# Kernel tuning notes

Hardware: AMD Instinct MI355X
Metric: run time of the kernel (lower is better)

The kernel has to match this reference:

```python
import jax, jax.numpy as jnp
import numpy as np

NUM_GRAPHS = 512
N_NODES = 131072
N_EDGES = 4194304
F_IN = 54
H_GCN = 16
H_LSTM = 32
N_CLASSES = 192
MAX_SEQ_LEN = 1024


def setup_inputs() -> dict:
    key = jax.random.key(0)
    ks = jax.random.split(key, 12)
    s = 0.1
    return {
        "x": jax.random.normal(ks[0], (N_NODES, F_IN), jnp.float32),
        "edge_index": jax.random.randint(ks[1], (2, N_EDGES), 0, N_NODES),
        "batch": jnp.sort(jax.random.randint(ks[2], (N_NODES,), 0, NUM_GRAPHS)),
        "gcn_w1": jax.random.normal(ks[3], (F_IN, H_GCN), jnp.float32) * s,
        "gcn_b1": jnp.zeros((H_GCN,), jnp.float32),
        "gcn_w2": jax.random.normal(ks[4], (H_GCN, H_GCN), jnp.float32) * s,
        "gcn_b2": jnp.zeros((H_GCN,), jnp.float32),
        "lstm0_wih": jax.random.normal(ks[5], (2, 4 * H_LSTM, H_GCN), jnp.float32) * s,
        "lstm0_whh": jax.random.normal(ks[6], (2, 4 * H_LSTM, H_LSTM), jnp.float32) * s,
        "lstm0_bih": jnp.zeros((2, 4 * H_LSTM), jnp.float32),
        "lstm0_bhh": jnp.zeros((2, 4 * H_LSTM), jnp.float32),
        "lstm1_wih": jax.random.normal(ks[7], (2, 4 * H_LSTM, 2 * H_LSTM), jnp.float32) * s,
        "lstm1_whh": jax.random.normal(ks[8], (2, 4 * H_LSTM, H_LSTM), jnp.float32) * s,
        "lstm1_bih": jnp.zeros((2, 4 * H_LSTM), jnp.float32),
        "lstm1_bhh": jnp.zeros((2, 4 * H_LSTM), jnp.float32),
        "fc_w": jax.random.normal(ks[9], (2 * H_LSTM, N_CLASSES), jnp.float32) * s,
        "fc_b": jnp.zeros((N_CLASSES,), jnp.float32),
        "max_seq_len": MAX_SEQ_LEN,
    }


def _lstm_dir(xseq, wih, whh, bih, bhh, reverse):
    # xseq: [B, T, D]; PyTorch gate order i, f, g, o.
    pre = jnp.einsum("btd,gd->btg", xseq, wih) + bih + bhh  # [B, T, 4H]
    B = xseq.shape[0]
    H = whh.shape[-1]

    def step(carry, g_t):
        h, c = carry
        g = g_t + h @ whh.T
        i, f, gg, o = jnp.split(g, 4, axis=-1)
        c = jax.nn.sigmoid(f) * c + jax.nn.sigmoid(i) * jnp.tanh(gg)
        h = jax.nn.sigmoid(o) * jnp.tanh(c)
        return (h, c), h

    init = (jnp.zeros((B, H), xseq.dtype), jnp.zeros((B, H), xseq.dtype))
    _, hs = jax.lax.scan(step, init, jnp.swapaxes(pre, 0, 1), reverse=reverse)
    return jnp.swapaxes(hs, 0, 1)  # [B, T, H]


def _bilstm(xseq, wih, whh, bih, bhh):
    fwd = _lstm_dir(xseq, wih[0], whh[0], bih[0], bhh[0], reverse=False)
    bwd = _lstm_dir(xseq, wih[1], whh[1], bih[1], bhh[1], reverse=True)
    return jnp.concatenate([fwd, bwd], axis=-1)


def reference(x, edge_index, batch, gcn_w1, gcn_b1, gcn_w2, gcn_b2,
              lstm0_wih, lstm0_whh, lstm0_bih, lstm0_bhh,
              lstm1_wih, lstm1_whh, lstm1_bih, lstm1_bhh,
              fc_w, fc_b, max_seq_len):
    N = x.shape[0]
    loop = jnp.arange(N)
    src = jnp.concatenate([edge_index[0], loop])  # GCNConv adds self-loops
    dst = jnp.concatenate([edge_index[1], loop])
    deg = jax.ops.segment_sum(jnp.ones_like(dst, jnp.float32), dst, num_segments=N)
    dinv = jax.lax.rsqrt(jnp.maximum(deg, 1.0))  # deg >= 1 due to self-loops
    norm = (dinv[src] * dinv[dst])[:, None]

    def conv(h, W, b):
        msg = (h @ W)[src] * norm
        return jax.ops.segment_sum(msg, dst, num_segments=N) + b

    h = jax.nn.relu(conv(x, gcn_w1, gcn_b1))
    # F.dropout(training=False) is identity in eval mode
    h = jax.nn.relu(conv(h, gcn_w2, gcn_b2))

    # Ragged -> padded [NUM_GRAPHS, max_seq_len, H_GCN] (batch is graph-sorted)
    counts = jax.ops.segment_sum(jnp.ones((N,), jnp.int32), batch, num_segments=NUM_GRAPHS)
    starts = jnp.concatenate([jnp.zeros((1,), jnp.int32), jnp.cumsum(counts)[:-1]])
    pos = jnp.arange(N) - starts[batch]
    padded = jnp.zeros((NUM_GRAPHS, max_seq_len, h.shape[1]), h.dtype).at[batch, pos].set(h, mode="drop")

    seq = _bilstm(padded, lstm0_wih, lstm0_whh, lstm0_bih, lstm0_bhh)
    seq = _bilstm(seq, lstm1_wih, lstm1_whh, lstm1_bih, lstm1_bhh)
    pooled = jnp.mean(seq, axis=1)  # mean over padded length, as in original
    return pooled @ fc_w + fc_b
```

## Files before the change

### kernel.cpp

```cpp
#include <hip/hip_runtime.h>
#include <cstdint>
#include <cstddef>

#define NG 512
#define NN 131072
#define NE 4194304
#define FIN 54
#define HG 16
#define HL 32
#define NC 192
#define TS 1024

#define NB 256
#define WH 512
#define EPW (NE/WH)

__device__ __forceinline__ float rcpf(float x){ return __builtin_amdgcn_rcpf(x); }
__device__ __forceinline__ float sigf(float x){ return rcpf(1.0f + __expf(-x)); }
__device__ __forceinline__ float tanhfast(float x){ return 1.0f - 2.0f*rcpf(__expf(2.0f*x) + 1.0f); }

__device__ __forceinline__ float4 uload4(const float* p){
  unsigned long long a = (unsigned long long)p;
  asm volatile("" : "+v"(a));
  return *(const float4*)a;
}

#define CEPS 1e-6f
#define HEPS 1e-6f

__global__ void k_initc(int* __restrict__ counts){
  counts[threadIdx.x] = 0;
}

__global__ void k_cnt(const int* __restrict__ batch, int* __restrict__ counts){
  int i = blockIdx.x*256 + threadIdx.x;
  if (i < NN) atomicAdd(&counts[batch[i]], 1);
}

__global__ void k_scan(const int* __restrict__ counts, int* __restrict__ starts){
  __shared__ int sc[NG];
  int t = threadIdx.x;
  sc[t] = counts[t]; __syncthreads();
  for (int off = 1; off < NG; off <<= 1){
    int v = (t >= off) ? sc[t-off] : 0;
    __syncthreads();
    sc[t] += v;
    __syncthreads();
  }
  starts[t] = sc[t] - counts[t];
}

__global__ void k_hist(const int* __restrict__ ei, int* __restrict__ hist){
  int w = blockIdx.x, tid = threadIdx.x;
  __shared__ int h[NB];
  h[tid] = 0;
  __syncthreads();
  int e0 = w*EPW;
  for (int i = tid; i < EPW; i += 256) atomicAdd(&h[ei[NE + e0 + i] >> 9], 1);
  __syncthreads();
  hist[tid*WH + w] = h[tid];
}

__global__ void k_scanH(const int* __restrict__ hist, int* __restrict__ offs,
                        int* __restrict__ bstart){
  __shared__ int tot[1024];
  int t = threadIdx.x;
  int base = t*128;
  int s = 0;
  for (int i = 0; i < 128; i++) s += hist[base + i];
  tot[t] = s; __syncthreads();
  for (int o = 1; o < 1024; o <<= 1){
    int v = (t >= o) ? tot[t-o] : 0;
    __syncthreads();
    tot[t] += v;
    __syncthreads();
  }
  int run = tot[t] - s;
  for (int i = 0; i < 128; i++){
    int idx = base + i;
    int h = hist[idx];
    offs[idx] = run;
    if ((idx & (WH-1)) == 0) bstart[idx / WH] = run;
    run += h;
  }
  if (t == 0) bstart[NB] = NE;
}

__global__ void k_binB(const int* __restrict__ ei, const int* __restrict__ offs,
                       uint2* __restrict__ pair){
  int w = blockIdx.x, tid = threadIdx.x;
  __shared__ int cur[NB];
  cur[tid] = offs[tid*WH + w];
  __syncthreads();
  int e0 = w*EPW;
  for (int i = tid; i < EPW; i += 256){
    int e = e0 + i;
    int s = ei[e], d = ei[NE + e];
    int b = d >> 9;
    int pos = atomicAdd(&cur[b], 1);
    pair[pos] = make_uint2((unsigned)s, (unsigned)(d & 511));
  }
}

__global__ void k_binC(const uint2* __restrict__ pair, const int* __restrict__ bstart,
                       int* __restrict__ eoff, int* __restrict__ ecnt, int* __restrict__ csr){
  int b = blockIdx.x, tid = threadIdx.x;
  __shared__ int h2[512];
  __shared__ int cur[512];
  h2[tid] = 0; h2[tid + 256] = 0;
  __syncthreads();
  int e0 = bstart[b], e1 = bstart[b+1];
  for (int i = e0 + tid; i < e1; i += 256) atomicAdd(&h2[pair[i].y], 1);
  __syncthreads();
  cur[tid] = h2[tid]; cur[tid + 256] = h2[tid + 256];
  __syncthreads();
  for (int o = 1; o < 256; o <<= 1){
    int v0 = (tid >= o) ? cur[tid - o] : 0;
    int v1 = (tid >= o) ? cur[256 + tid - o] : 0;
    __syncthreads();
    cur[tid] += v0; cur[256 + tid] += v1;
    __syncthreads();
  }
  int half0 = cur[255];
  __syncthreads();
  cur[256 + tid] += half0;
  __syncthreads();
  int n0 = tid, n1 = tid + 256;
  int ex0 = cur[n0] - h2[n0];
  int ex1 = cur[n1] - h2[n1];
  eoff[b*512 + n0] = e0 + ex0; ecnt[b*512 + n0] = h2[n0];
  eoff[b*512 + n1] = e0 + ex1; ecnt[b*512 + n1] = h2[n1];
  __syncthreads();
  cur[n0] = e0 + ex0; cur[n1] = e0 + ex1;
  __syncthreads();
  for (int i = e0 + tid; i < e1; i += 256){
    uint2 u = pair[i];
    int pos = atomicAdd(&cur[u.y], 1);
    csr[pos] = (int)u.x;
  }
}

__global__ void k_dinv(const int* __restrict__ ecnt, float* __restrict__ dinv){
  int i = blockIdx.x*256 + threadIdx.x;
  if (i < NN) dinv[i] = 1.0f / sqrtf((float)(ecnt[i] + 1));
}

__global__ void k_lin1(const float* __restrict__ x, const float* __restrict__ w1,
                       float* __restrict__ xa){
  __shared__ float w[FIN*HG];
  __shared__ float xs[16][FIN+2];
  int tid = threadIdx.x;
  for (int i = tid; i < FIN*HG; i += 256) w[i] = w1[i];
  const float4* gx = (const float4*)(x + (size_t)blockIdx.x*16*FIN);
  if (tid < 216){
    float4 v4 = gx[tid];
    int fi = tid*4;
#pragma unroll
    for (int e = 0; e < 4; e++){
      int idx = fi + e;
      xs[idx/FIN][idx%FIN] = ((const float*)&v4)[e];
    }
  }
  __syncthreads();
  int node = tid >> 4, f = tid & 15;
  const float* xr = xs[node];
  float acc = 0.0f;
#pragma unroll
  for (int k = 0; k < FIN; k++) acc = fmaf(xr[k], w[k*HG + f], acc);
  xa[((size_t)blockIdx.x*16 + node)*HG + f] = acc;
}

__global__ void k_gather(const float* __restrict__ v, const int* __restrict__ csr,
                         const int* __restrict__ eoff, const int* __restrict__ ecnt,
                         const float* __restrict__ dinv, const float* __restrict__ bias,
                         int dorelu, float* __restrict__ out){
  int gid = blockIdx.x*16 + (threadIdx.x >> 4);
  int f = threadIdx.x & 15;
  float dv = dinv[gid];
  float a0 = v[(size_t)gid*HG + f] * dv, a1 = 0.0f, a2 = 0.0f, a3 = 0.0f;
  int o = eoff[gid], n = ecnt[gid];
  int i = 0;
  for (; i + 8 <= n; i += 8){
    int s0 = csr[o+i],   s1 = csr[o+i+1], s2 = csr[o+i+2], s3 = csr[o+i+3];
    int s4 = csr[o+i+4], s5 = csr[o+i+5], s6 = csr[o+i+6], s7 = csr[o+i+7];
    a0 = fmaf(v[(size_t)s0*HG + f], dinv[s0], a0);
    a1 = fmaf(v[(size_t)s1*HG + f], dinv[s1], a1);
    a2 = fmaf(v[(size_t)s2*HG + f], dinv[s2], a2);
    a3 = fmaf(v[(size_t)s3*HG + f], dinv[s3], a3);
    a0 = fmaf(v[(size_t)s4*HG + f], dinv[s4], a0);
    a1 = fmaf(v[(size_t)s5*HG + f], dinv[s5], a1);
    a2 = fmaf(v[(size_t)s6*HG + f], dinv[s6], a2);
    a3 = fmaf(v[(size_t)s7*HG + f], dinv[s7], a3);
  }
  for (; i + 4 <= n; i += 4){
    int s0 = csr[o+i], s1 = csr[o+i+1], s2 = csr[o+i+2], s3 = csr[o+i+3];
    a0 = fmaf(v[(size_t)s0*HG + f], dinv[s0], a0);
    a1 = fmaf(v[(size_t)s1*HG + f], dinv[s1], a1);
    a2 = fmaf(v[(size_t)s2*HG + f], dinv[s2], a2);
    a3 = fmaf(v[(size_t)s3*HG + f], dinv[s3], a3);
  }
  for (; i < n; i++){
    int s = csr[o+i];
    a0 = fmaf(v[(size_t)s*HG + f], dinv[s], a0);
  }
  float acc = ((a0 + a1) + (a2 + a3)) * dv;
  if (dorelu) acc = fmaxf(acc + bias[f], 0.0f);
  out[(size_t)gid*HG + f] = acc;
}

__global__ void k_relu_lin(const float* __restrict__ agg, const float* __restrict__ b1,
                           const float* __restrict__ w2, float* __restrict__ hb){
  __shared__ float w[HG*HG];
  __shared__ float bb[HG];
  int tid = threadIdx.x;
  if (tid < HG*HG) w[tid] = w2[tid];
  if (tid < HG) bb[tid] = b1[tid];
  __syncthreads();
  int id = blockIdx.x*256 + tid;
  if (id >= NN*HG) return;
  int node = id >> 4, f = id & 15;
  const float* ar = agg + (size_t)node*HG;
  float acc = 0.0f;
#pragma unroll
  for (int k = 0; k < HG; k++){
    float h = fmaxf(ar[k] + bb[k], 0.0f);
    acc = fmaf(h, w[k*HG + f], acc);
  }
  hb[id] = acc;
}


__global__ __launch_bounds__(64, 1) void k_lstm0(
    const float* __restrict__ h2in, const int* __restrict__ starts, const int* __restrict__ counts,
    const float* __restrict__ wih, const float* __restrict__ whh,
    const float* __restrict__ bih, const float* __restrict__ bhh,
    float* __restrict__ out0, int* __restrict__ tconv, int* __restrict__ az)
{
  const int g = blockIdx.x >> 1, dir = blockIdx.x & 1;
  const int lane = threadIdx.x;
  const int j = lane & 31, half = lane >> 5;
  const int rA = (half ? 32 : 0) + j;
  const int rB = rA + 64;
  float wxA[HG], wxB[HG], whA[HL], whB[HL];
  { const float* a = wih + ((size_t)dir*128 + rA)*HG;
    const float* b = wih + ((size_t)dir*128 + rB)*HG;
#pragma unroll
    for (int k = 0; k < HG; k++){ wxA[k] = a[k]; wxB[k] = b[k]; }
    const float* ua = whh + ((size_t)dir*128 + rA)*HL;
    const float* ub = whh + ((size_t)dir*128 + rB)*HL;
#pragma unroll
    for (int k = 0; k < HL; k++){ whA[k] = ua[k]; whB[k] = ub[k]; }
  }
  const float pbA = bih[dir*128 + rA] + bhh[dir*128 + rA];
  const float pbB = bih[dir*128 + rB] + bhh[dir*128 + rB];
  int cnt = counts[g]; if (cnt > TS) cnt = TS;
  const int s0 = starts[g];
  float* outg = out0 + (size_t)g*TS*64 + dir*32;

  __shared__ __align__(16) float hbuf[HL];

  unsigned long long bz = __ballot((pbA == 0.0f) && (pbB == 0.0f));
  bool allzero = (bz == ~0ull);
  if (dir == 1 && lane == 0) az[0] = allzero ? 1 : 0;
  if (!half) hbuf[j] = 0.0f;

  int t0, dt; bool skipall = false;
  if (dir == 0){ t0 = 0; dt = 1; }
  else if (allzero){
    t0 = cnt - 1; dt = -1;
    if (t0 < 0) skipall = true;
  } else { t0 = TS - 1; dt = -1; }

  float c = 0.0f, h = 0.0f; bool fwdconv = false;
  float4 X[4]; int t = t0;

  if (!skipall){
    if (cnt > 0){
      int ta = t0 < 0 ? 0 : (t0 > cnt-1 ? cnt-1 : t0);
      const float* pa = h2in + (size_t)(s0 + ta)*HG;
#pragma unroll
      for (int q = 0; q < 4; q++) X[q] = uload4(pa + 4*q);
    }
    for (;;){
      float a0 = pbA, a1 = 0.0f, a2 = 0.0f, a3 = 0.0f;
      float b0 = pbB, b1 = 0.0f, b2 = 0.0f, b3 = 0.0f;
      if (t < cnt){
#pragma unroll
        for (int q = 0; q < 4; q++){ float4 xq = X[q];
          a0 = fmaf(xq.x, wxA[4*q+0], a0); a1 = fmaf(xq.y, wxA[4*q+1], a1);
          a2 = fmaf(xq.z, wxA[4*q+2], a2); a3 = fmaf(xq.w, wxA[4*q+3], a3);
          b0 = fmaf(xq.x, wxB[4*q+0], b0); b1 = fmaf(xq.y, wxB[4*q+1], b1);
          b2 = fmaf(xq.z, wxB[4*q+2], b2); b3 = fmaf(xq.w, wxB[4*q+3], b3); }
      }
      { int tp = t + dt;
        if (tp >= 0 && tp < cnt){
          const float* pp = h2in + (size_t)(s0 + tp)*HG;
#pragma unroll
          for (int q = 0; q < 4; q++) X[q] = uload4(pp + 4*q);
        } }
      { const float4* h4 = (const float4*)hbuf;
#pragma unroll
        for (int q = 0; q < HL/4; q++){ float4 hq = h4[q];
          a0 = fmaf(hq.x, whA[4*q+0], a0); a1 = fmaf(hq.y, whA[4*q+1], a1);
          a2 = fmaf(hq.z, whA[4*q+2], a2); a3 = fmaf(hq.w, whA[4*q+3], a3);
          b0 = fmaf(hq.x, whB[4*q+0], b0); b1 = fmaf(hq.y, whB[4*q+1], b1);
          b2 = fmaf(hq.z, whB[4*q+2], b2); b3 = fmaf(hq.w, whB[4*q+3], b3); }
      }
      float uA = (a0 + a1) + (a2 + a3);
      float uB = (b0 + b1) + (b2 + b3);
      float aA = sigf(uA);
      float ub2 = half ? uB : (uB + uB);
      float sv = sigf(ub2);
      float aB = half ? sv : (sv + sv - 1.0f);
      float pq = aA*aB;
      float part = __shfl_xor(half ? aA : pq, 32);
      float f_ = half ? aA : part;
      float p_ = half ? part : pq;
      float cn = fmaf(f_, c, p_);
      float th = tanhfast(cn);
      float ov = __shfl_xor(aB, 32);
      float o_ = half ? aB : ov;
      float hn = o_ * th;
      bool eq = (fabsf(cn - c) <= CEPS*(1.0f + fabsf(cn))) && (fabsf(hn - h) <= HEPS);
      c = cn; h = hn;
      unsigned long long m = __ballot(eq);
      if (!half) hbuf[j] = h;
      if (half) outg[(size_t)t*64 + j] = h;
      if (dir == 0 && t >= cnt + 1 && m == ~0ull){
        if (lane == 0) tconv[g] = t - 1;
        fwdconv = true;
        break;
      }
      t += dt;
      if (dir == 0){ if (t >= TS) break; } else { if (t < 0) break; }
    }
  }
  if (dir == 0 && !fwdconv && lane == 0) tconv[g] = TS;
}

__global__ __launch_bounds__(64, 1) void k_lstm1(
    const float* __restrict__ gl0, const int* __restrict__ tconv,
    const int* __restrict__ counts, const int* __restrict__ az,
    const float* __restrict__ wih, const float* __restrict__ whh,
    const float* __restrict__ bih, const float* __restrict__ bhh,
    float* __restrict__ pooled)
{
  const int g = blockIdx.x >> 1, dir = blockIdx.x & 1;
  const int lane = threadIdx.x;
  const int j = lane & 31, half = lane >> 5;
  const int rA = (half ? 32 : 0) + j, rB = rA + 64;
  float wxA[64], wxB[64], whA[HL], whB[HL];
  { const float4* A4 = (const float4*)(wih + ((size_t)dir*128 + rA)*64);
    const float4* B4 = (const float4*)(wih + ((size_t)dir*128 + rB)*64);
#pragma unroll
    for (int k = 0; k < 16; k++){ ((float4*)wxA)[k] = A4[k]; ((float4*)wxB)[k] = B4[k]; }
    const float4* a4 = (const float4*)(whh + ((size_t)dir*128 + rA)*HL);
    const float4* b4 = (const float4*)(whh + ((size_t)dir*128 + rB)*HL);
#pragma unroll
    for (int k = 0; k < 8; k++){ ((float4*)whA)[k] = a4[k]; ((float4*)whB)[k] = b4[k]; }
  }
  const float pbA = bih[dir*128 + rA] + bhh[dir*128 + rA];
  const float pbB = bih[dir*128 + rB] + bhh[dir*128 + rB];
  const float* gin = gl0 + (size_t)g*TS*64;
  const int tcv = tconv[g];
  int cnt = counts[g]; if (cnt > TS) cnt = TS;
  const bool mz = (az[0] != 0) && (half != 0);

  __shared__ __align__(16) float hbuf[HL];
  __shared__ __align__(16) float xrow[2][64];

  if (!half) hbuf[j] = 0.0f;

  float c = 0.0f, h = 0.0f, hsum = 0.0f;

#define L1_GATES(XPTR) \
  float a0 = pbA, a1 = 0.0f, a2 = 0.0f, a3 = 0.0f; \
  float b0 = pbB, b1 = 0.0f, b2 = 0.0f, b3 = 0.0f; \
  { const float4* xp_ = (const float4*)(XPTR); \
    _Pragma("unroll") \
    for (int q = 0; q < 16; q++){ float4 xq = xp_[q]; \
      a0 = fmaf(xq.x, wxA[4*q+0], a0); a1 = fmaf(xq.y, wxA[4*q+1], a1); \
      a2 = fmaf(xq.z, wxA[4*q+2], a2); a3 = fmaf(xq.w, wxA[4*q+3], a3); \
      b0 = fmaf(xq.x, wxB[4*q+0], b0); b1 = fmaf(xq.y, wxB[4*q+1], b1); \
      b2 = fmaf(xq.z, wxB[4*q+2], b2); b3 = fmaf(xq.w, wxB[4*q+3], b3); } }

#define L1_HFMA() \
  { const float4* h4_ = (const float4*)hbuf; \
    _Pragma("unroll") \
    for (int q = 0; q < HL/4; q++){ float4 hq = h4_[q]; \
      a0 = fmaf(hq.x, whA[4*q+0], a0); a1 = fmaf(hq.y, whA[4*q+1], a1); \
      a2 = fmaf(hq.z, whA[4*q+2], a2); a3 = fmaf(hq.w, whA[4*q+3], a3); \
      b0 = fmaf(hq.x, whB[4*q+0], b0); b1 = fmaf(hq.y, whB[4*q+1], b1); \
      b2 = fmaf(hq.z, whB[4*q+2], b2); b3 = fmaf(hq.w, whB[4*q+3], b3); } }

#define L1_TAIL() \
  float uA = (a0 + a1) + (a2 + a3); \
  float uB = (b0 + b1) + (b2 + b3); \
  float aA = sigf(uA); \
  float ub2 = half ? uB : (uB + uB); \
  float sv = sigf(ub2); \
  float aB = half ? sv : (sv + sv - 1.0f); \
  float pq = aA*aB; \
  float part = __shfl_xor(half ? aA : pq, 32); \
  float f_ = half ? aA : part; \
  float p_ = half ? part : pq; \
  float cn = fmaf(f_, c, p_); \
  float th = tanhfast(cn); \
  float ov = __shfl_xor(aB, 32); \
  float o_ = half ? aB : ov; \
  float hn = o_ * th; \
  bool eq = (fabsf(cn - c) <= CEPS*(1.0f + fabsf(cn))) && (fabsf(hn - h) <= HEPS); \
  c = cn; h = hn; hsum += h; \
  if (!half) hbuf[j] = h;

  if (dir == 0){
    const int tend = (tcv < TS-1) ? tcv : TS-1;
    { float xv0 = gin[lane];
      if (mz && 0 >= cnt) xv0 = 0.0f;
      xrow[0][lane] = xv0; }
    float xv = gin[(size_t)1*64 + lane];
    int ph = 0;
    for (int t = 0; t <= tend; t++){
      L1_GATES(xrow[ph]);
      { int tn = t + 1; float xw = (mz && tn >= cnt) ? 0.0f : xv;
        xrow[ph^1][lane] = xw; }
      { int tp = t + 2; if (tp > TS-1) tp = TS-1;
        xv = gin[(size_t)tp*64 + lane]; }
      L1_HFMA();
      L1_TAIL(); (void)eq;
      ph ^= 1;
    }
    if (tcv < TS-1){
      float xc0 = pbA, xc1 = 0.0f, xc2 = 0.0f, xc3 = 0.0f;
      float yc0 = pbB, yc1 = 0.0f, yc2 = 0.0f, yc3 = 0.0f;
      { const float4* xp = (const float4*)xrow[ph];
#pragma unroll
        for (int q = 0; q < 16; q++){ float4 xq = xp[q];
          xc0 = fmaf(xq.x, wxA[4*q+0], xc0); xc1 = fmaf(xq.y, wxA[4*q+1], xc1);
          xc2 = fmaf(xq.z, wxA[4*q+2], xc2); xc3 = fmaf(xq.w, wxA[4*q+3], xc3);
          yc0 = fmaf(xq.x, wxB[4*q+0], yc0); yc1 = fmaf(xq.y, wxB[4*q+1], yc1);
          yc2 = fmaf(xq.z, wxB[4*q+2], yc2); yc3 = fmaf(xq.w, wxB[4*q+3], yc3); } }
      for (int t = tcv+1; t < TS; t++){
        float a0 = xc0, a1 = xc1, a2 = xc2, a3 = xc3;
        float b0 = yc0, b1 = yc1, b2 = yc2, b3 = yc3;
        L1_HFMA();
        L1_TAIL();
        unsigned long long m = __ballot(eq);
        if (m == ~0ull){ hsum += h * (float)(TS-1 - t); break; }
      }
    }
  } else {
    int tfull;
    if (tcv + 1 <= TS - 1){
      { float xv0 = gin[(size_t)(tcv+1)*64 + lane];
        if (mz && tcv+1 >= cnt) xv0 = 0.0f;
        xrow[0][lane] = xv0; }
      float xc0 = pbA, xc1 = 0.0f, xc2 = 0.0f, xc3 = 0.0f;
      float yc0 = pbB, yc1 = 0.0f, yc2 = 0.0f, yc3 = 0.0f;
      { const float4* xp = (const float4*)xrow[0];
#pragma unroll
        for (int q = 0; q < 16; q++){ float4 xq = xp[q];
          xc0 = fmaf(xq.x, wxA[4*q+0], xc0); xc1 = fmaf(xq.y, wxA[4*q+1], xc1);
          xc2 = fmaf(xq.z, wxA[4*q+2], xc2); xc3 = fmaf(xq.w, wxA[4*q+3], xc3);
          yc0 = fmaf(xq.x, wxB[4*q+0], yc0); yc1 = fmaf(xq.y, wxB[4*q+1], yc1);
          yc2 = fmaf(xq.z, wxB[4*q+2], yc2); yc3 = fmaf(xq.w, wxB[4*q+3], yc3); } }
      int t = TS - 1; bool jumped = false;
      for (; t >= tcv + 1; t--){
        float a0 = xc0, a1 = xc1, a2 = xc2, a3 = xc3;
        float b0 = yc0, b1 = yc1, b2 = yc2, b3 = yc3;
        L1_HFMA();
        L1_TAIL();
        unsigned long long m = __ballot(eq);
        if (m == ~0ull){ hsum += h * (float)(t - tcv); jumped = true; break; }
      }
      tfull = jumped ? (tcv - 1) : tcv;
    } else tfull = TS - 1;
    if (tfull >= 0){
      { float xv0 = gin[(size_t)tfull*64 + lane];
        if (mz && tfull >= cnt) xv0 = 0.0f;
        xrow[0][lane] = xv0; }
      float xv; { int tp = tfull - 1; if (tp < 0) tp = 0;
        xv = gin[(size_t)tp*64 + lane]; }
      int ph = 0;
      for (int t = tfull; t >= 0; t--){
        L1_GATES(xrow[ph]);
        { int tn = t - 1; float xw = (mz && tn >= cnt) ? 0.0f : xv;
          xrow[ph^1][lane] = xw; }
        { int tp = t - 2; if (tp < 0) tp = 0;
          xv = gin[(size_t)tp*64 + lane]; }
        L1_HFMA();
        L1_TAIL(); (void)eq;
        ph ^= 1;
      }
    }
  }
  if (!half) pooled[(size_t)g*64 + dir*32 + j] = hsum * (1.0f/(float)TS);
#undef L1_GATES
#undef L1_HFMA
#undef L1_TAIL
}

__global__ void k_fc(const float* __restrict__ pooled, const float* __restrict__ fcw,
                     const float* __restrict__ fcb, float* __restrict__ out){
  __shared__ float p[64];
  int g = blockIdx.x, cix = threadIdx.x;
  if (cix < 64) p[cix] = pooled[(size_t)g*64 + cix];
  __syncthreads();
  float acc = fcb[cix];
#pragma unroll
  for (int k = 0; k < 64; k++) acc = fmaf(p[k], fcw[k*NC + cix], acc);
  out[(size_t)g*NC + cix] = acc;
}

extern "C" void kernel_launch(void* const* d_in, const int* in_sizes, int n_in,
                              void* d_out, int out_size, void* d_ws, size_t ws_size,
                              hipStream_t stream) {
  const float* x        = (const float*)d_in[0];
  const int*   ei       = (const int*)  d_in[1];
  const int*   batch    = (const int*)  d_in[2];
  const float* gcn_w1   = (const float*)d_in[3];
  const float* gcn_b1   = (const float*)d_in[4];
  const float* gcn_w2   = (const float*)d_in[5];
  const float* gcn_b2   = (const float*)d_in[6];
  const float* l0_wih   = (const float*)d_in[7];
  const float* l0_whh   = (const float*)d_in[8];
  const float* l0_bih   = (const float*)d_in[9];
  const float* l0_bhh   = (const float*)d_in[10];
  const float* l1_wih   = (const float*)d_in[11];
  const float* l1_whh   = (const float*)d_in[12];
  const float* l1_bih   = (const float*)d_in[13];
  const float* l1_bhh   = (const float*)d_in[14];
  const float* fc_w     = (const float*)d_in[15];
  const float* fc_b     = (const float*)d_in[16];
  float* out = (float*)d_out;

  float* ws   = (float*)d_ws;
  float* B0   = ws;
  float* B1   = B0 + (size_t)NN*HG;
  float* B2   = B1 + (size_t)NN*HG;
  float* dinv = B2 + (size_t)NN*HG;
  int*   ecnt   = (int*)(dinv + NN);
  int*   eoff   = ecnt + NN;
  int*   hist   = eoff + NN;
  int*   offs   = hist + NB*WH;
  int*   counts = offs + NB*WH;
  int*   starts = counts + NG;
  int*   tconv  = starts + NG;
  int*   bstart = tconv + NG;
  int*   az     = bstart + NB + 4;
  float* pooled = (float*)(bstart + NB + 64);
  int*   csr    = (int*)(pooled + (size_t)NG*64);
  float* out0   = (float*)(csr + (size_t)NE);
  uint2* pair   = (uint2*)out0;
  size_t needed = ((size_t)((float*)out0 - ws) + (size_t)NG*TS*64) * sizeof(float);
  if (ws_size < needed) return;

  k_initc <<<1, NG, 0, stream>>>(counts);
  k_cnt   <<<NN/256, 256, 0, stream>>>(batch, counts);
  k_hist  <<<WH, 256, 0, stream>>>(ei, hist);
  k_scanH <<<1, 1024, 0, stream>>>(hist, offs, bstart);
  k_scan  <<<1, NG, 0, stream>>>(counts, starts);
  k_binB  <<<WH, 256, 0, stream>>>(ei, offs, pair);
  k_binC  <<<NB, 256, 0, stream>>>(pair, bstart, eoff, ecnt, csr);
  k_dinv  <<<NN/256, 256, 0, stream>>>(ecnt, dinv);
  k_lin1  <<<NN/16, 256, 0, stream>>>(x, gcn_w1, B0);
  k_gather<<<(NN*HG)/256, 256, 0, stream>>>(B0, csr, eoff, ecnt, dinv, gcn_b2, 0, B1);
  k_relu_lin<<<(NN*HG)/256, 256, 0, stream>>>(B1, gcn_b1, gcn_w2, B2);
  k_gather<<<(NN*HG)/256, 256, 0, stream>>>(B2, csr, eoff, ecnt, dinv, gcn_b2, 1, B1);
  k_lstm0 <<<NG*2, 64, 0, stream>>>(B1, starts, counts, l0_wih, l0_whh, l0_bih, l0_bhh, out0, tconv, az);
  k_lstm1 <<<NG*2, 64, 0, stream>>>(out0, tconv, counts, az, l1_wih, l1_whh, l1_bih, l1_bhh, pooled);
  k_fc    <<<NG, NC, 0, stream>>>(pooled, fc_w, fc_b, out);
}
```

Baseline: 1.005 ms.

## Deepen input prefetch and split LSTM loops into padded/valid phases

The layer-0 LSTM loop is split into separate phases for padded and valid timesteps. This removes per-step branches on t<cnt, and the valid phase is unrolled four times with a four-deep rotating register prefetch of input rows. The hidden state is now read back from shared memory into registers right after each store rather than at the start of the next step, and the weights are loaded as float4. Layer 1 prefetches inputs three steps ahead instead of one, hiding global-load latency on the serial recurrence at the cost of more registers and code size.

```diff
diff --git a/kernel.cpp b/kernel.cpp
--- a/kernel.cpp
+++ b/kernel.cpp
@@ -24,6 +24,7 @@
   asm volatile("" : "+v"(a));
   return *(const float4*)a;
 }
+
 
 #define CEPS 1e-6f
 #define HEPS 1e-6f
@@ -230,6 +231,23 @@
 }
 
 
+#define LTAIL() \
+  float uA = (a0 + a1) + (a2 + a3); \
+  float uB = (b0 + b1) + (b2 + b3); \
+  float aA = sigf(uA); \
+  float ub2 = half ? uB : (uB + uB); \
+  float sv = sigf(ub2); \
+  float aB = half ? sv : (sv + sv - 1.0f); \
+  float pq = aA*aB; \
+  float part = __shfl_xor(half ? aA : pq, 32); \
+  float f_ = half ? aA : part; \
+  float p_ = half ? part : pq; \
+  float cn = fmaf(f_, c, p_); \
+  float th = tanhfast(cn); \
+  float ov = __shfl_xor(aB, 32); \
+  float o_ = half ? aB : ov; \
+  float hn = o_ * th;
+
 __global__ __launch_bounds__(64, 1) void k_lstm0(
     const float* __restrict__ h2in, const int* __restrict__ starts, const int* __restrict__ counts,
     const float* __restrict__ wih, const float* __restrict__ whh,
@@ -242,14 +260,14 @@
   const int rA = (half ? 32 : 0) + j;
   const int rB = rA + 64;
   float wxA[HG], wxB[HG], whA[HL], whB[HL];
-  { const float* a = wih + ((size_t)dir*128 + rA)*HG;
-    const float* b = wih + ((size_t)dir*128 + rB)*HG;
-#pragma unroll
-    for (int k = 0; k < HG; k++){ wxA[k] = a[k]; wxB[k] = b[k]; }
-    const float* ua = whh + ((size_t)dir*128 + rA)*HL;
-    const float* ub = whh + ((size_t)dir*128 + rB)*HL;
-#pragma unroll
-    for (int k = 0; k < HL; k++){ whA[k] = ua[k]; whB[k] = ub[k]; }
+  { const float4* a4 = (const float4*)(wih + ((size_t)dir*128 + rA)*HG);
+    const float4* b4 = (const float4*)(wih + ((size_t)dir*128 + rB)*HG);
+#pragma unroll
+    for (int k = 0; k < HG/4; k++){ ((float4*)wxA)[k] = a4[k]; ((float4*)wxB)[k] = b4[k]; }
+    const float4* ua4 = (const float4*)(whh + ((size_t)dir*128 + rA)*HL);
+    const float4* ub4 = (const float4*)(whh + ((size_t)dir*128 + rB)*HL);
+#pragma unroll
+    for (int k = 0; k < HL/4; k++){ ((float4*)whA)[k] = ua4[k]; ((float4*)whB)[k] = ub4[k]; }
   }
   const float pbA = bih[dir*128 + rA] + bhh[dir*128 + rA];
   const float pbB = bih[dir*128 + rB] + bhh[dir*128 + rB];
@@ -263,79 +281,100 @@
   bool allzero = (bz == ~0ull);
   if (dir == 1 && lane == 0) az[0] = allzero ? 1 : 0;
   if (!half) hbuf[j] = 0.0f;
-
-  int t0, dt; bool skipall = false;
-  if (dir == 0){ t0 = 0; dt = 1; }
-  else if (allzero){
-    t0 = cnt - 1; dt = -1;
-    if (t0 < 0) skipall = true;
-  } else { t0 = TS - 1; dt = -1; }
-
-  float c = 0.0f, h = 0.0f; bool fwdconv = false;
-  float4 X[4]; int t = t0;
-
-  if (!skipall){
-    if (cnt > 0){
-      int ta = t0 < 0 ? 0 : (t0 > cnt-1 ? cnt-1 : t0);
-      const float* pa = h2in + (size_t)(s0 + ta)*HG;
-#pragma unroll
-      for (int q = 0; q < 4; q++) X[q] = uload4(pa + 4*q);
-    }
-    for (;;){
+  float4 H[8];
+  { const float4* h4r = (const float4*)hbuf;
+#pragma unroll
+    for (int q = 0; q < 8; q++) H[q] = h4r[q]; }
+
+  float c = 0.0f, h = 0.0f;
+  int t, dt, tendF;
+
+#define L0_HFMA() \
+  _Pragma("unroll") \
+  for (int q = 0; q < 8; q++){ float4 hq = H[q]; \
+    a0 = fmaf(hq.x, whA[4*q+0], a0); a1 = fmaf(hq.y, whA[4*q+1], a1); \
+    a2 = fmaf(hq.z, whA[4*q+2], a2); a3 = fmaf(hq.w, whA[4*q+3], a3); \
+    b0 = fmaf(hq.x, whB[4*q+0], b0); b1 = fmaf(hq.y, whB[4*q+1], b1); \
+    b2 = fmaf(hq.z, whB[4*q+2], b2); b3 = fmaf(hq.w, whB[4*q+3], b3); }
+
+#define L0_STORE() \
+  c = cn; h = hn; \
+  if (!half) hbuf[j] = h; \
+  { const float4* h4r = (const float4*)hbuf; \
+    _Pragma("unroll") for (int q = 0; q < 8; q++) H[q] = h4r[q]; } \
+  if (half) outg[(size_t)t*64 + j] = h;
+
+#define L0_F(P) { \
+  if (t == tendF) goto l0_fdone; \
+  float a0 = pbA, a1 = 0.0f, a2 = 0.0f, a3 = 0.0f; \
+  float b0 = pbB, b1 = 0.0f, b2 = 0.0f, b3 = 0.0f; \
+  _Pragma("unroll") \
+  for (int q = 0; q < 4; q++){ float4 xq = XR##P[q]; \
+    a0 = fmaf(xq.x, wxA[4*q+0], a0); a1 = fmaf(xq.y, wxA[4*q+1], a1); \
+    a2 = fmaf(xq.z, wxA[4*q+2], a2); a3 = fmaf(xq.w, wxA[4*q+3], a3); \
+    b0 = fmaf(xq.x, wxB[4*q+0], b0); b1 = fmaf(xq.y, wxB[4*q+1], b1); \
+    b2 = fmaf(xq.z, wxB[4*q+2], b2); b3 = fmaf(xq.w, wxB[4*q+3], b3); } \
+  { int tp = t + 4*dt; tp = tp < 0 ? 0 : (tp > cnt-1 ? cnt-1 : tp); \
+    const float* pp = h2in + (size_t)(s0 + tp)*HG; \
+    XR##P[0] = uload4(pp); XR##P[1] = uload4(pp+4); \
+    XR##P[2] = uload4(pp+8); XR##P[3] = uload4(pp+12); } \
+  L0_HFMA(); \
+  LTAIL(); \
+  L0_STORE(); \
+  t += dt; }
+
+  if (dir == 1 && !allzero){
+    for (t = TS - 1; t >= cnt; t--){
       float a0 = pbA, a1 = 0.0f, a2 = 0.0f, a3 = 0.0f;
       float b0 = pbB, b1 = 0.0f, b2 = 0.0f, b3 = 0.0f;
-      if (t < cnt){
-#pragma unroll
-        for (int q = 0; q < 4; q++){ float4 xq = X[q];
-          a0 = fmaf(xq.x, wxA[4*q+0], a0); a1 = fmaf(xq.y, wxA[4*q+1], a1);
-          a2 = fmaf(xq.z, wxA[4*q+2], a2); a3 = fmaf(xq.w, wxA[4*q+3], a3);
-          b0 = fmaf(xq.x, wxB[4*q+0], b0); b1 = fmaf(xq.y, wxB[4*q+1], b1);
-          b2 = fmaf(xq.z, wxB[4*q+2], b2); b3 = fmaf(xq.w, wxB[4*q+3], b3); }
-      }
-      { int tp = t + dt;
-        if (tp >= 0 && tp < cnt){
-          const float* pp = h2in + (size_t)(s0 + tp)*HG;
-#pragma unroll
-          for (int q = 0; q < 4; q++) X[q] = uload4(pp + 4*q);
-        } }
-      { const float4* h4 = (const float4*)hbuf;
-#pragma unroll
-        for (int q = 0; q < HL/4; q++){ float4 hq = h4[q];
-          a0 = fmaf(hq.x, whA[4*q+0], a0); a1 = fmaf(hq.y, whA[4*q+1], a1);
-          a2 = fmaf(hq.z, whA[4*q+2], a2); a3 = fmaf(hq.w, whA[4*q+3], a3);
-          b0 = fmaf(hq.x, whB[4*q+0], b0); b1 = fmaf(hq.y, whB[4*q+1], b1);
-          b2 = fmaf(hq.z, whB[4*q+2], b2); b3 = fmaf(hq.w, whB[4*q+3], b3); }
-      }
-      float uA = (a0 + a1) + (a2 + a3);
-      float uB = (b0 + b1) + (b2 + b3);
-      float aA = sigf(uA);
-      float ub2 = half ? uB : (uB + uB);
-      float sv = sigf(ub2);
-      float aB = half ? sv : (sv + sv - 1.0f);
-      float pq = aA*aB;
-      float part = __shfl_xor(half ? aA : pq, 32);
-      float f_ = half ? aA : part;
-      float p_ = half ? part : pq;
-      float cn = fmaf(f_, c, p_);
-      float th = tanhfast(cn);
-      float ov = __shfl_xor(aB, 32);
-      float o_ = half ? aB : ov;
-      float hn = o_ * th;
+      L0_HFMA();
+      LTAIL();
+      L0_STORE();
+    }
+  }
+
+  if (cnt > 0){
+    if (dir == 0){ t = 0; dt = 1; tendF = cnt; }
+    else { t = cnt - 1; dt = -1; tendF = -1; }
+    float4 XR0[4], XR1[4], XR2[4], XR3[4];
+    { int r1 = t + dt, r2 = t + 2*dt, r3 = t + 3*dt;
+      r1 = r1 < 0 ? 0 : (r1 > cnt-1 ? cnt-1 : r1);
+      r2 = r2 < 0 ? 0 : (r2 > cnt-1 ? cnt-1 : r2);
+      r3 = r3 < 0 ? 0 : (r3 > cnt-1 ? cnt-1 : r3);
+      const float* p0 = h2in + (size_t)(s0 + t)*HG;
+      const float* p1 = h2in + (size_t)(s0 + r1)*HG;
+      const float* p2 = h2in + (size_t)(s0 + r2)*HG;
+      const float* p3 = h2in + (size_t)(s0 + r3)*HG;
+      XR0[0]=uload4(p0); XR0[1]=uload4(p0+4); XR0[2]=uload4(p0+8); XR0[3]=uload4(p0+12);
+      XR1[0]=uload4(p1); XR1[1]=uload4(p1+4); XR1[2]=uload4(p1+8); XR1[3]=uload4(p1+12);
+      XR2[0]=uload4(p2); XR2[1]=uload4(p2+4); XR2[2]=uload4(p2+8); XR2[3]=uload4(p2+12);
+      XR3[0]=uload4(p3); XR3[1]=uload4(p3+4); XR3[2]=uload4(p3+8); XR3[3]=uload4(p3+12);
+    }
+    for (;;){ L0_F(0); L0_F(1); L0_F(2); L0_F(3); }
+l0_fdone: ;
+  }
+
+  if (dir == 0){
+    bool fwdconv = false;
+    for (t = cnt; t < TS; t++){
+      float a0 = pbA, a1 = 0.0f, a2 = 0.0f, a3 = 0.0f;
+      float b0 = pbB, b1 = 0.0f, b2 = 0.0f, b3 = 0.0f;
+      L0_HFMA();
+      LTAIL();
       bool eq = (fabsf(cn - c) <= CEPS*(1.0f + fabsf(cn))) && (fabsf(hn - h) <= HEPS);
-      c = cn; h = hn;
+      L0_STORE();
       unsigned long long m = __ballot(eq);
-      if (!half) hbuf[j] = h;
-      if (half) outg[(size_t)t*64 + j] = h;
-      if (dir == 0 && t >= cnt + 1 && m == ~0ull){
+      if (t >= cnt + 1 && m == ~0ull){
         if (lane == 0) tconv[g] = t - 1;
         fwdconv = true;
         break;
       }
-      t += dt;
-      if (dir == 0){ if (t >= TS) break; } else { if (t < 0) break; }
     }
-  }
-  if (dir == 0 && !fwdconv && lane == 0) tconv[g] = TS;
+    if (!fwdconv && lane == 0) tconv[g] = TS;
+  }
+#undef L0_F
+#undef L0_STORE
+#undef L0_HFMA
 }
 
 __global__ __launch_bounds__(64, 1) void k_lstm1(
@@ -393,41 +432,27 @@
       b0 = fmaf(hq.x, whB[4*q+0], b0); b1 = fmaf(hq.y, whB[4*q+1], b1); \
       b2 = fmaf(hq.z, whB[4*q+2], b2); b3 = fmaf(hq.w, whB[4*q+3], b3); } }
 
-#define L1_TAIL() \
-  float uA = (a0 + a1) + (a2 + a3); \
-  float uB = (b0 + b1) + (b2 + b3); \
-  float aA = sigf(uA); \
-  float ub2 = half ? uB : (uB + uB); \
-  float sv = sigf(ub2); \
-  float aB = half ? sv : (sv + sv - 1.0f); \
-  float pq = aA*aB; \
-  float part = __shfl_xor(half ? aA : pq, 32); \
-  float f_ = half ? aA : part; \
-  float p_ = half ? part : pq; \
-  float cn = fmaf(f_, c, p_); \
-  float th = tanhfast(cn); \
-  float ov = __shfl_xor(aB, 32); \
-  float o_ = half ? aB : ov; \
-  float hn = o_ * th; \
-  bool eq = (fabsf(cn - c) <= CEPS*(1.0f + fabsf(cn))) && (fabsf(hn - h) <= HEPS); \
+#define L1_STORE() \
   c = cn; h = hn; hsum += h; \
   if (!half) hbuf[j] = h;
 
   if (dir == 0){
     const int tend = (tcv < TS-1) ? tcv : TS-1;
-    { float xv0 = gin[lane];
-      if (mz && 0 >= cnt) xv0 = 0.0f;
-      xrow[0][lane] = xv0; }
-    float xv = gin[(size_t)1*64 + lane];
+    { float x0 = gin[lane];
+      if (mz && 0 >= cnt) x0 = 0.0f;
+      xrow[0][lane] = x0; }
+    float v1 = gin[64 + lane], v2 = gin[128 + lane], v3 = gin[192 + lane];
     int ph = 0;
     for (int t = 0; t <= tend; t++){
       L1_GATES(xrow[ph]);
-      { int tn = t + 1; float xw = (mz && tn >= cnt) ? 0.0f : xv;
+      { int tn = t + 1; float xw = (mz && tn >= cnt) ? 0.0f : v1;
         xrow[ph^1][lane] = xw; }
-      { int tp = t + 2; if (tp > TS-1) tp = TS-1;
-        xv = gin[(size_t)tp*64 + lane]; }
+      v1 = v2; v2 = v3;
+      { int tp = t + 4; if (tp > TS-1) tp = TS-1;
+        v3 = gin[(size_t)tp*64 + lane]; }
       L1_HFMA();
-      L1_TAIL(); (void)eq;
+      LTAIL();
+      L1_STORE();
       ph ^= 1;
     }
     if (tcv < TS-1){
@@ -444,7 +469,9 @@
         float a0 = xc0, a1 = xc1, a2 = xc2, a3 = xc3;
         float b0 = yc0, b1 = yc1, b2 = yc2, b3 = yc3;
         L1_HFMA();
-        L1_TAIL();
+        LTAIL();
+        bool eq = (fabsf(cn - c) <= CEPS*(1.0f + fabsf(cn))) && (fabsf(hn - h) <= HEPS);
+        L1_STORE();
         unsigned long long m = __ballot(eq);
         if (m == ~0ull){ hsum += h * (float)(TS-1 - t); break; }
       }
@@ -452,9 +479,9 @@
   } else {
     int tfull;
     if (tcv + 1 <= TS - 1){
-      { float xv0 = gin[(size_t)(tcv+1)*64 + lane];
-        if (mz && tcv+1 >= cnt) xv0 = 0.0f;
-        xrow[0][lane] = xv0; }
+      { float x0 = gin[(size_t)(tcv+1)*64 + lane];
+        if (mz && tcv+1 >= cnt) x0 = 0.0f;
+        xrow[0][lane] = x0; }
       float xc0 = pbA, xc1 = 0.0f, xc2 = 0.0f, xc3 = 0.0f;
       float yc0 = pbB, yc1 = 0.0f, yc2 = 0.0f, yc3 = 0.0f;
       { const float4* xp = (const float4*)xrow[0];
@@ -469,27 +496,35 @@
         float a0 = xc0, a1 = xc1, a2 = xc2, a3 = xc3;
         float b0 = yc0, b1 = yc1, b2 = yc2, b3 = yc3;
         L1_HFMA();
-        L1_TAIL();
+        LTAIL();
+        bool eq = (fabsf(cn - c) <= CEPS*(1.0f + fabsf(cn))) && (fabsf(hn - h) <= HEPS);
+        L1_STORE();
         unsigned long long m = __ballot(eq);
         if (m == ~0ull){ hsum += h * (float)(t - tcv); jumped = true; break; }
       }
       tfull = jumped ? (tcv - 1) : tcv;
     } else tfull = TS - 1;
     if (tfull >= 0){
-      { float xv0 = gin[(size_t)tfull*64 + lane];
-        if (mz && tfull >= cnt) xv0 = 0.0f;
-        xrow[0][lane] = xv0; }
-      float xv; { int tp = tfull - 1; if (tp < 0) tp = 0;
-        xv = gin[(size_t)tp*64 + lane]; }
+      { float x0 = gin[(size_t)tfull*64 + lane];
+        if (mz && tfull >= cnt) x0 = 0.0f;
+        xrow[0][lane] = x0; }
+      int r1 = tfull-1 < 0 ? 0 : tfull-1;
+      int r2 = tfull-2 < 0 ? 0 : tfull-2;
+      int r3 = tfull-3 < 0 ? 0 : tfull-3;
+      float v1 = gin[(size_t)r1*64 + lane];
+      float v2 = gin[(size_t)r2*64 + lane];
+      float v3 = gin[(size_t)r3*64 + lane];
       int ph = 0;
       for (int t = tfull; t >= 0; t--){
         L1_GATES(xrow[ph]);
-        { int tn = t - 1; float xw = (mz && tn >= cnt) ? 0.0f : xv;
+        { int tn = t - 1; float xw = (mz && tn >= cnt) ? 0.0f : v1;
           xrow[ph^1][lane] = xw; }
-        { int tp = t - 2; if (tp < 0) tp = 0;
-          xv = gin[(size_t)tp*64 + lane]; }
+        v1 = v2; v2 = v3;
+        { int tp = t - 4; if (tp < 0) tp = 0;
+          v3 = gin[(size_t)tp*64 + lane]; }
         L1_HFMA();
-        L1_TAIL(); (void)eq;
+        LTAIL();
+        L1_STORE();
         ph ^= 1;
       }
     }
@@ -497,7 +532,7 @@
   if (!half) pooled[(size_t)g*64 + dir*32 + j] = hsum * (1.0f/(float)TS);
 #undef L1_GATES
 #undef L1_HFMA
-#undef L1_TAIL
+#undef L1_STORE
 }
 
 __global__ void k_fc(const float* __restrict__ pooled, const float* __restrict__ fcw,
```

Measured after the change: 949.3 us. 5.6% less time.
